# Kernel optimization log

Hardware: AMD Instinct MI355X
Metric: run time of the kernel (lower is better)

The kernel has to match this reference:

```python
import jax, jax.numpy as jnp
import numpy as np

B, S, O = 65536, 32, 16  # batch, state_dim, observation_dim


def setup_inputs() -> dict:
    key = jax.random.key(0)
    k1, k2, k3, k4 = jax.random.split(key, 4)
    observation = jax.random.normal(k1, (B, O), dtype=jnp.float32)
    # SPD observation noise covariance per batch element
    L = 0.1 * jax.random.normal(k2, (B, O, O), dtype=jnp.float32)
    observation_noise = jnp.einsum('bij,bkj->bik', L, L) + 1e-3 * jnp.eye(O, dtype=jnp.float32)
    observation_matrix = 0.001 * jax.random.normal(k3, (O, S), dtype=jnp.float32)
    observation_bias = 1e-6 * jax.random.normal(k4, (O,), dtype=jnp.float32)
    prior_mean = jnp.zeros((S,), dtype=jnp.float32)
    prior_precision = jnp.eye(S, dtype=jnp.float32)
    return {
        'observation': observation,
        'observation_noise': observation_noise,
        'observation_matrix': observation_matrix,
        'observation_bias': observation_bias,
        'prior_mean': prior_mean,
        'prior_precision': prior_precision,
    }


def reference(observation, observation_noise, observation_matrix, observation_bias,
              prior_mean, prior_precision):
    # observation: [B, O]; observation_noise: [B, O, O]
    noise_prec = jnp.linalg.inv(observation_noise)                      # [B, O, O]
    HtR = jnp.einsum('os,bop->bsp', observation_matrix, noise_prec)     # H^T R^{-1}: [B, S, O]
    innovation_cov = jnp.einsum('bso,ot->bst', HtR, observation_matrix) # [B, S, S]
    posterior_covariance = jnp.linalg.inv(prior_precision + innovation_cov)  # [B, S, S]
    residual = jnp.einsum('bso,bo->bs', HtR, observation - observation_bias)[..., None]  # [B, S, 1]
    prior_term = (prior_precision @ prior_mean)[:, None]                # [S, 1]
    posterior_mean = posterior_covariance @ (prior_term + residual)     # [B, S, 1]
    return posterior_mean, posterior_covariance
```

## Files before the change

kernel.cpp:

```cpp
#include <hip/hip_runtime.h>
#include <hip/hip_bf16.h>


typedef __attribute__((ext_vector_type(8))) short bf16x8;
typedef __attribute__((ext_vector_type(4))) float f32x4;

__device__ __forceinline__ unsigned bf16rne(float f) {
    unsigned x = __float_as_uint(f);
    return (x + 0x7FFFu + ((x >> 16) & 1u)) >> 16;
}
__device__ __forceinline__ unsigned pack2(float a, float b) {
    return bf16rne(a) | (bf16rne(b) << 16);
}

__global__ void lgs_setup(const float* __restrict__ H, const float* __restrict__ bias,
                          const float* __restrict__ mu0, const float* __restrict__ P,
                          float* __restrict__ ws)
{
    __shared__ float pinv[32][33];
    __shared__ float Gsh[16][33];
    const int l = threadIdx.x;

    float m[32];
#pragma unroll
    for (int i = 0; i < 32; ++i)
        m[i] = (l < 32) ? P[i * 32 + l] : ((i == (l - 32)) ? 1.0f : 0.0f);

#pragma unroll
    for (int k = 0; k < 32; ++k) {
        float bc[32];
#pragma unroll
        for (int i = 0; i < 32; ++i) bc[i] = __shfl(m[i], k, 64);
        float a = m[k] * (1.0f / bc[k]);
#pragma unroll
        for (int i = 0; i < 32; ++i)
            if (i != k) m[i] -= bc[i] * a;
        m[k] = a;
    }
    if (l >= 32) {
        const int c = l - 32;
#pragma unroll
        for (int i = 0; i < 32; ++i) pinv[c][i] = m[i];
    }
    asm volatile("" ::: "memory");

    for (int idx = l; idx < 512; idx += 64) {
        int o = idx >> 5, s = idx & 31;
        float acc = 0.f;
        for (int u = 0; u < 32; ++u) acc += H[o * 32 + u] * pinv[s][u];
        Gsh[o][s] = acc;
    }
    asm volatile("" ::: "memory");

    for (int idx = l; idx < 256; idx += 64) {
        int j = idx >> 4, i = idx & 15;
        float acc = 0.f;
        for (int s = 0; s < 32; ++s) acc += Gsh[i][s] * H[j * 32 + s];
        ws[idx] = acc;
    }
    unsigned* wsu = (unsigned*)ws;
    for (int idx = l; idx < 512; idx += 64) {
        int r = idx >> 8, rem = idx & 255;
        int ll = rem >> 2, j = rem & 3;
        int mm = 16 * r + (ll & 15);
        int kb = (((ll >> 4) * 8) + 2 * j) & 15;
        wsu[768 + idx] = pack2(-0.5f * Gsh[kb][mm], -0.5f * Gsh[kb + 1][mm]);
    }
    for (int idx = l; idx < 1024; idx += 64) {
        int tt = idx >> 8, rem = idx & 255;
        int ll = rem >> 2, j = rem & 3;
        int row = 16 * (tt >> 1) + ((ll >> 4) << 2) + j;
        int col = 16 * (tt & 1) + (ll & 15);
        ws[1280 + idx] = pinv[col][row];
    }
    for (int idx = l; idx < 512; idx += 64) {
        int c = idx >> 8, rem = idx & 255;
        int ll = rem >> 2, j2 = rem & 3;
        int col = 16 * c + (ll & 15);
        int k = (((ll >> 4) * 8) + 2 * j2) & 15;
        wsu[2304 + idx] = pack2(0.5f * Gsh[k][col], 0.5f * Gsh[k + 1][col]);
    }
    if (l < 16) {
        float acc = bias[l];
        for (int s = 0; s < 32; ++s) acc += H[l * 32 + s] * mu0[s];
        ws[2816 + l] = acc;
    }
    if (l < 32) ws[2832 + l] = mu0[l];
}

#define BCAST16(x, K) __int_as_float(__builtin_amdgcn_ds_swizzle(__float_as_int(x), (((K) << 5) | 0x10)))

template <int K>
__device__ __forceinline__ void gj16(int t, float (&m)[16], float (&v)[16])
{
    if (t == K) m[K] = 1.0f / m[K];
    float bc[16];
#pragma unroll
    for (int i = 0; i < 16; ++i) bc[i] = BCAST16(m[i], K);
    float pk = m[K] * bc[K];
#pragma unroll
    for (int i = 0; i < 16; ++i)
        if (i != K) m[i] -= bc[i] * pk;
    m[K] = pk;
    float a = v[K] * bc[K];
#pragma unroll
    for (int i = 0; i < 16; ++i)
        if (i != K) v[i] -= bc[i] * a;
    v[K] = a;
}

__global__ __launch_bounds__(512, 5) void lgs_main(
    const float* __restrict__ obs, const float* __restrict__ noise,
    const float* __restrict__ ws,
    float* __restrict__ out_mean, float* __restrict__ out_cov, int B)
{
    __shared__ float ld[8192];

    const int tid  = threadIdx.x;
    const int l    = tid & 63;
    const int t    = tid & 15;
    const int slot = tid >> 4;
    const int wv   = tid >> 6;
    const int b    = blockIdx.x * 32 + slot;
    const int bb   = (b < B) ? b : (B - 1);

    const float* __restrict__ Acm  = ws;
    const float* __restrict__ cvec = ws + 2816;
    const float* __restrict__ m0v  = ws + 2832;

    float m[16], v[16];

    const float4* Rr = (const float4*)(noise + (size_t)bb * 256 + t * 16);
    const float4* Ar = (const float4*)(Acm + t * 16);
#pragma unroll
    for (int i = 0; i < 4; ++i) {
        float4 r = Rr[i], a = Ar[i];
        m[4*i+0] = r.x + a.x; m[4*i+1] = r.y + a.y;
        m[4*i+2] = r.z + a.z; m[4*i+3] = r.w + a.w;
    }
#pragma unroll
    for (int i = 0; i < 16; ++i) v[i] = (i == t) ? 1.0f : 0.0f;

    gj16<0>(t, m, v);   gj16<1>(t, m, v);   gj16<2>(t, m, v);   gj16<3>(t, m, v);
    gj16<4>(t, m, v);   gj16<5>(t, m, v);   gj16<6>(t, m, v);   gj16<7>(t, m, v);
    gj16<8>(t, m, v);   gj16<9>(t, m, v);   gj16<10>(t, m, v);  gj16<11>(t, m, v);
    gj16<12>(t, m, v);  gj16<13>(t, m, v);  gj16<14>(t, m, v);  gj16<15>(t, m, v);

    {
        const int xw = t & 3;
        float* wb = &ld[slot * 256 + t * 16];
        *(float4*)&wb[(0 ^ xw) << 2] = make_float4(v[0],  v[1],  v[2],  v[3]);
        *(float4*)&wb[(1 ^ xw) << 2] = make_float4(v[4],  v[5],  v[6],  v[7]);
        *(float4*)&wb[(2 ^ xw) << 2] = make_float4(v[8],  v[9],  v[10], v[11]);
        *(float4*)&wb[(3 ^ xw) << 2] = make_float4(v[12], v[13], v[14], v[15]);
    }

    const uint4*  AF4 = (const uint4*)(ws + 768);
    const uint4*  BG4 = (const uint4*)(ws + 2304);
    const float4* PF4 = (const float4*)(ws + 1280);
    uint4 a0u = AF4[l], a1u = AF4[64 + l];
    uint4 g0u = BG4[l], g1u = BG4[64 + l];
    bf16x8 A0, A1, Bg0, Bg1;
    __builtin_memcpy(&A0,  &a0u, 16);
    __builtin_memcpy(&A1,  &a1u, 16);
    __builtin_memcpy(&Bg0, &g0u, 16);
    __builtin_memcpy(&Bg1, &g1u, 16);

    const int ch = l & 15;
    const int gp = l >> 4;
    const int gq = (gp & 1) * 2;
    const int xq = ch & 3;
    const int xt = (ch & 1) << 2;
    const float4 cv = ((const float4*)cvec)[gp];
    const float mu0a = m0v[ch], mu0b = m0v[16 + ch];
    const f32x4 zero = {0.f, 0.f, 0.f, 0.f};

#pragma unroll
    for (int h = 0; h < 4; ++h) {
        const int sh  = wv * 4 + h;
        const int bh  = blockIdx.x * 32 + sh;
        const int bhc = (bh < B) ? bh : (B - 1);

        const float* qb = &ld[sh * 256 + ch * 16];
        float4 qa = *(const float4*)&qb[((gq    ) ^ xq) << 2];
        float4 qc = *(const float4*)&qb[((gq + 1) ^ xq) << 2];
        unsigned qarr[4] = { pack2(qa.x, qa.y), pack2(qa.z, qa.w),
                             pack2(qc.x, qc.y), pack2(qc.z, qc.w) };
        bf16x8 Qa; __builtin_memcpy(&Qa, qarr, 16);
        f32x4 d0 = __builtin_amdgcn_mfma_f32_16x16x32_bf16(Qa, Bg0, zero, 0, 0, 0);
        f32x4 d1 = __builtin_amdgcn_mfma_f32_16x16x32_bf16(Qa, Bg1, zero, 0, 0, 0);

        float4 yv = *(const float4*)(obs + (size_t)bhc * 16 + gp * 4);
        float z0 = yv.x - cv.x, z1 = yv.y - cv.y, z2 = yv.z - cv.z, z3 = yv.w - cv.w;
        float p0 = d0[0]*z0 + d0[1]*z1 + d0[2]*z2 + d0[3]*z3;
        float p1 = d1[0]*z0 + d1[1]*z1 + d1[2]*z2 + d1[3]*z3;
        p0 += __int_as_float(__builtin_amdgcn_ds_swizzle(__float_as_int(p0), 0x401F));
        p1 += __int_as_float(__builtin_amdgcn_ds_swizzle(__float_as_int(p1), 0x401F));
        p0 += __shfl_xor(p0, 32, 64);
        p1 += __shfl_xor(p1, 32, 64);
        if (bh < B) {
            if (gp == 0) out_mean[(size_t)bh * 32 + ch]      = mu0a + p0;
            if (gp == 1) out_mean[(size_t)bh * 32 + 16 + ch] = mu0b + p1;
        }

        unsigned* tb = (unsigned*)&ld[sh * 256];
        const int g2 = gp * 2;
        *(uint2*)&tb[      ch * 8 + (g2 ^ xt)] =
            make_uint2(pack2(d0[0], d0[1]), pack2(d0[2], d0[3]));
        *(uint2*)&tb[128 + ch * 8 + (g2 ^ xt)] =
            make_uint2(pack2(d1[0], d1[1]), pack2(d1[2], d1[3]));

        const int kp = (gp & 1) * 4;
        uint4 bu0 = *(const uint4*)&tb[      ch * 8 + (kp ^ xt)];
        uint4 bu1 = *(const uint4*)&tb[128 + ch * 8 + (kp ^ xt)];
        bf16x8 Bf0, Bf1;
        __builtin_memcpy(&Bf0, &bu0, 16);
        __builtin_memcpy(&Bf1, &bu1, 16);

        float4 pq0 = PF4[l];
        float4 pq1 = PF4[64 + l];
        float4 pq2 = PF4[128 + l];
        float4 pq3 = PF4[192 + l];
        f32x4 pfr0; pfr0[0]=pq0.x; pfr0[1]=pq0.y; pfr0[2]=pq0.z; pfr0[3]=pq0.w;
        f32x4 pfr1; pfr1[0]=pq1.x; pfr1[1]=pq1.y; pfr1[2]=pq1.z; pfr1[3]=pq1.w;
        f32x4 pfr2; pfr2[0]=pq2.x; pfr2[1]=pq2.y; pfr2[2]=pq2.z; pfr2[3]=pq2.w;
        f32x4 pfr3; pfr3[0]=pq3.x; pfr3[1]=pq3.y; pfr3[2]=pq3.z; pfr3[3]=pq3.w;
        f32x4 s00 = __builtin_amdgcn_mfma_f32_16x16x32_bf16(A0, Bf0, pfr0, 0, 0, 0);
        f32x4 s01 = __builtin_amdgcn_mfma_f32_16x16x32_bf16(A0, Bf1, pfr1, 0, 0, 0);
        f32x4 s10 = __builtin_amdgcn_mfma_f32_16x16x32_bf16(A1, Bf0, pfr2, 0, 0, 0);
        f32x4 s11 = __builtin_amdgcn_mfma_f32_16x16x32_bf16(A1, Bf1, pfr3, 0, 0, 0);

        if (bh < B) {
            float* Sb = out_cov + (size_t)bh * 1024 + (gp * 4) * 32 + ch;
#pragma unroll
            for (int j = 0; j < 4; ++j) {
                Sb[j * 32]       = s00[j];
                Sb[j * 32 + 16]  = s01[j];
                Sb[j * 32 + 512] = s10[j];
                Sb[j * 32 + 528] = s11[j];
            }
        }
    }
}

extern "C" void kernel_launch(void* const* d_in, const int* in_sizes, int n_in,
                              void* d_out, int out_size, void* d_ws, size_t ws_size,
                              hipStream_t stream)
{
    const float* obs   = (const float*)d_in[0];
    const float* noise = (const float*)d_in[1];
    const float* H     = (const float*)d_in[2];
    const float* bias  = (const float*)d_in[3];
    const float* mu0   = (const float*)d_in[4];
    const float* P     = (const float*)d_in[5];
    float* ws = (float*)d_ws;

    const int B = in_sizes[0] / 16;
    float* out_mean = (float*)d_out;
    float* out_cov  = out_mean + (size_t)B * 32;

    lgs_setup<<<1, 64, 0, stream>>>(H, bias, mu0, P, ws);
    lgs_main<<<(B + 31) / 32, 512, 0, stream>>>(obs, noise, ws, out_mean, out_cov, B);
}
```

Baseline: 110.8 us.

## Process two batch groups per block, interleaving second inversion with first epilogue

```diff
diff --git a/kernel.cpp b/kernel.cpp
--- a/kernel.cpp
+++ b/kernel.cpp
@@ -109,7 +109,14 @@
     v[K] = a;
 }
 
-__global__ __launch_bounds__(512, 5) void lgs_main(
+template <int S>
+__device__ __forceinline__ void gj4(int t, float (&m)[16], float (&v)[16])
+{
+    gj16<S>(t, m, v);  gj16<S + 1>(t, m, v);
+    gj16<S + 2>(t, m, v);  gj16<S + 3>(t, m, v);
+}
+
+__global__ __launch_bounds__(512, 4) void lgs_main(
     const float* __restrict__ obs, const float* __restrict__ noise,
     const float* __restrict__ ws,
     float* __restrict__ out_mean, float* __restrict__ out_cov, int B)
@@ -121,50 +128,18 @@
     const int t    = tid & 15;
     const int slot = tid >> 4;
     const int wv   = tid >> 6;
-    const int b    = blockIdx.x * 32 + slot;
-    const int bb   = (b < B) ? b : (B - 1);
+    const int b0   = blockIdx.x * 64;
+    const int bA   = b0 + slot;
+    const int bB   = b0 + 32 + slot;
+    const int bbA  = (bA < B) ? bA : (B - 1);
+    const int bbB  = (bB < B) ? bB : (B - 1);
 
     const float* __restrict__ Acm  = ws;
     const float* __restrict__ cvec = ws + 2816;
     const float* __restrict__ m0v  = ws + 2832;
-
-    float m[16], v[16];
-
-    const float4* Rr = (const float4*)(noise + (size_t)bb * 256 + t * 16);
-    const float4* Ar = (const float4*)(Acm + t * 16);
-#pragma unroll
-    for (int i = 0; i < 4; ++i) {
-        float4 r = Rr[i], a = Ar[i];
-        m[4*i+0] = r.x + a.x; m[4*i+1] = r.y + a.y;
-        m[4*i+2] = r.z + a.z; m[4*i+3] = r.w + a.w;
-    }
-#pragma unroll
-    for (int i = 0; i < 16; ++i) v[i] = (i == t) ? 1.0f : 0.0f;
-
-    gj16<0>(t, m, v);   gj16<1>(t, m, v);   gj16<2>(t, m, v);   gj16<3>(t, m, v);
-    gj16<4>(t, m, v);   gj16<5>(t, m, v);   gj16<6>(t, m, v);   gj16<7>(t, m, v);
-    gj16<8>(t, m, v);   gj16<9>(t, m, v);   gj16<10>(t, m, v);  gj16<11>(t, m, v);
-    gj16<12>(t, m, v);  gj16<13>(t, m, v);  gj16<14>(t, m, v);  gj16<15>(t, m, v);
-
-    {
-        const int xw = t & 3;
-        float* wb = &ld[slot * 256 + t * 16];
-        *(float4*)&wb[(0 ^ xw) << 2] = make_float4(v[0],  v[1],  v[2],  v[3]);
-        *(float4*)&wb[(1 ^ xw) << 2] = make_float4(v[4],  v[5],  v[6],  v[7]);
-        *(float4*)&wb[(2 ^ xw) << 2] = make_float4(v[8],  v[9],  v[10], v[11]);
-        *(float4*)&wb[(3 ^ xw) << 2] = make_float4(v[12], v[13], v[14], v[15]);
-    }
-
     const uint4*  AF4 = (const uint4*)(ws + 768);
     const uint4*  BG4 = (const uint4*)(ws + 2304);
     const float4* PF4 = (const float4*)(ws + 1280);
-    uint4 a0u = AF4[l], a1u = AF4[64 + l];
-    uint4 g0u = BG4[l], g1u = BG4[64 + l];
-    bf16x8 A0, A1, Bg0, Bg1;
-    __builtin_memcpy(&A0,  &a0u, 16);
-    __builtin_memcpy(&A1,  &a1u, 16);
-    __builtin_memcpy(&Bg0, &g0u, 16);
-    __builtin_memcpy(&Bg1, &g1u, 16);
 
     const int ch = l & 15;
     const int gp = l >> 4;
@@ -173,13 +148,36 @@
     const int xt = (ch & 1) << 2;
     const float4 cv = ((const float4*)cvec)[gp];
     const float mu0a = m0v[ch], mu0b = m0v[16 + ch];
-    const f32x4 zero = {0.f, 0.f, 0.f, 0.f};
-
-#pragma unroll
-    for (int h = 0; h < 4; ++h) {
+
+    auto loadM = [&](float (&mm)[16], int bbx) {
+        const float4* Rr = (const float4*)(noise + (size_t)bbx * 256 + t * 16);
+        const float4* Ar = (const float4*)(Acm + t * 16);
+#pragma unroll
+        for (int i = 0; i < 4; ++i) {
+            float4 r = Rr[i], a = Ar[i];
+            mm[4*i+0] = r.x + a.x; mm[4*i+1] = r.y + a.y;
+            mm[4*i+2] = r.z + a.z; mm[4*i+3] = r.w + a.w;
+        }
+    };
+    auto stageQ = [&](const float (&vv)[16]) {
+        const int xw = t & 3;
+        float* wb = &ld[slot * 256 + t * 16];
+        *(float4*)&wb[(0 ^ xw) << 2] = make_float4(vv[0],  vv[1],  vv[2],  vv[3]);
+        *(float4*)&wb[(1 ^ xw) << 2] = make_float4(vv[4],  vv[5],  vv[6],  vv[7]);
+        *(float4*)&wb[(2 ^ xw) << 2] = make_float4(vv[8],  vv[9],  vv[10], vv[11]);
+        *(float4*)&wb[(3 ^ xw) << 2] = make_float4(vv[12], vv[13], vv[14], vv[15]);
+    };
+
+    auto epi = [&](int h, int ofs) {
         const int sh  = wv * 4 + h;
-        const int bh  = blockIdx.x * 32 + sh;
+        const int bh  = b0 + ofs + sh;
         const int bhc = (bh < B) ? bh : (B - 1);
+        const f32x4 zero = {0.f, 0.f, 0.f, 0.f};
+
+        uint4 g0u = BG4[l], g1u = BG4[64 + l];
+        bf16x8 Bg0, Bg1;
+        __builtin_memcpy(&Bg0, &g0u, 16);
+        __builtin_memcpy(&Bg1, &g1u, 16);
 
         const float* qb = &ld[sh * 256 + ch * 16];
         float4 qa = *(const float4*)&qb[((gq    ) ^ xq) << 2];
@@ -217,6 +215,10 @@
         __builtin_memcpy(&Bf0, &bu0, 16);
         __builtin_memcpy(&Bf1, &bu1, 16);
 
+        uint4 a0u = AF4[l], a1u = AF4[64 + l];
+        bf16x8 A0, A1;
+        __builtin_memcpy(&A0, &a0u, 16);
+        __builtin_memcpy(&A1, &a1u, 16);
         float4 pq0 = PF4[l];
         float4 pq1 = PF4[64 + l];
         float4 pq2 = PF4[128 + l];
@@ -240,7 +242,27 @@
                 Sb[j * 32 + 528] = s11[j];
             }
         }
-    }
+    };
+
+    float m[16], v[16];
+    loadM(m, bbA);
+#pragma unroll
+    for (int i = 0; i < 16; ++i) v[i] = (i == t) ? 1.0f : 0.0f;
+    gj4<0>(t, m, v);  gj4<4>(t, m, v);  gj4<8>(t, m, v);  gj4<12>(t, m, v);
+    stageQ(v);
+
+    float m2[16], v2[16];
+    loadM(m2, bbB);
+#pragma unroll
+    for (int i = 0; i < 16; ++i) v2[i] = (i == t) ? 1.0f : 0.0f;
+
+    gj4<0>(t, m2, v2);   epi(0, 0);
+    gj4<4>(t, m2, v2);   epi(1, 0);
+    gj4<8>(t, m2, v2);   epi(2, 0);
+    gj4<12>(t, m2, v2);  epi(3, 0);
+
+    stageQ(v2);
+    epi(0, 32);  epi(1, 32);  epi(2, 32);  epi(3, 32);
 }
 
 extern "C" void kernel_launch(void* const* d_in, const int* in_sizes, int n_in,
@@ -260,5 +282,5 @@
     float* out_cov  = out_mean + (size_t)B * 32;
 
     lgs_setup<<<1, 64, 0, stream>>>(H, bias, mu0, P, ws);
-    lgs_main<<<(B + 31) / 32, 512, 0, stream>>>(obs, noise, ws, out_mean, out_cov, B);
-}
+    lgs_main<<<(B + 63) / 64, 512, 0, stream>>>(obs, noise, ws, out_mean, out_cov, B);
+}
```

Result: slower. 414.8 us (+274.2%).
